# Optimization experiments

Measured on AMD Instinct MI355X. Metric: run time of the kernel, lower is better.

## Reference

```python
import jax, jax.numpy as jnp
import numpy as np

SCALE = 2.0   # init scale
OFFSET = 0.5  # init offset
BIG = 1e10    # stand-in for +inf so grads stay finite
N_PAD = 2048  # number of zero-padded pc columns per sample


def setup_inputs() -> dict:
    key = jax.random.key(0)
    k1, k2 = jax.random.split(key)
    vertices = jax.random.normal(k1, (4, 3, 64, 32, 64), dtype=jnp.float32)
    pc = jax.random.normal(k2, (4, 3, 8192), dtype=jnp.float32)
    # zero-pad the tail columns, mimicking variable-length point clouds
    pc = pc.at[:, :, 8192 - N_PAD:].set(0.0)
    return {"vertices": vertices, "pc": pc}


def _chamfer_loss(v, p, mask):
    # v: [N,3] mesh-top points; p: [M,3] cloud points; mask: [M] valid flags
    # squared pairwise distances via ||v||^2 + ||p||^2 - 2 v.p
    d = (jnp.sum(v * v, axis=1)[:, None]
         + jnp.sum(p * p, axis=1)[None, :]
         - 2.0 * (v @ p.T))                      # [N, M]
    dist1 = jnp.min(jnp.where(mask[None, :], d, BIG), axis=1)  # [N] v -> nearest valid p
    dist2 = jnp.min(d, axis=0)                                  # [M] p -> nearest v
    n_valid = jnp.maximum(jnp.sum(mask), 1).astype(d.dtype)
    return jnp.mean(dist1) + jnp.sum(jnp.where(mask, dist2, 0.0)) / n_valid


def reference(vertices, pc):
    B = vertices.shape[0]
    # top surface: last index along dim 3, flattened -> [B, 3, N]
    top = vertices[:, :, :, -1, :].reshape(B, 3, -1)
    top = (top - OFFSET) * SCALE
    v = jnp.transpose(top, (0, 2, 1))   # [B, N, 3]
    p = jnp.transpose(pc, (0, 2, 1))    # [B, M, 3]
    mask = ~jnp.all(pc == 0.0, axis=1)  # [B, M] valid (non-zero-padded) points
    loss = jax.vmap(_chamfer_loss)(v, p, mask)  # [B]
    return jnp.mean(loss)
```

## Files before the change

kernel.cpp:

```cpp
#include <hip/hip_runtime.h>

#define BATCH   4
#define NPTS    4096
#define MPTS    8192
#define TPB     256
#define VPT     8
#define MSPLIT  32
#define NSPLIT  16
#define MLEN    (MPTS / MSPLIT)
#define NLEN    (NPTS / NSPLIT)
#define D1_NBLK (NPTS / (TPB * VPT))
#define D2_MBLK (MPTS / (TPB * VPT))
#define D1_BLOCKS (BATCH * D1_NBLK * MSPLIT)
#define D2_BLOCKS (BATCH * D2_MBLK * NSPLIT)
#define BIGF    1.0e30f

#define PART1_ELEMS (MSPLIT * BATCH * NPTS)
#define PART2_ELEMS (NSPLIT * BATCH * MPTS)

#define R1_BLOCKS ((BATCH * NPTS) / (TPB * 4))
#define R2_BLOCKS ((BATCH * MPTS) / (TPB * 4))
#define R_BLOCKS  (R1_BLOCKS + R2_BLOCKS)

#define CTRL_FLOATS 16

__device__ __forceinline__ float vtop(const float* __restrict__ v, int b, int c, int n) {
    return v[b * 393216 + c * 131072 + ((n >> 6) << 11) + 1984 + (n & 63)];
}

__global__ void __launch_bounds__(TPB) dist_kernel(const float* __restrict__ vert,
                                                   const float* __restrict__ pc,
                                                   float* __restrict__ part1,
                                                   float* __restrict__ part2,
                                                   float* __restrict__ ctrl) {
    __shared__ float4 tile[TPB];
    const int tid = threadIdx.x;
    int blk = blockIdx.x;

    if (blk == 0 && tid < CTRL_FLOATS) ctrl[tid] = 0.0f;

    if (blk < D1_BLOCKS) {
        const int c  = blk % MSPLIT;
        const int nb = (blk / MSPLIT) % D1_NBLK;
        const int b  = blk / (MSPLIT * D1_NBLK);
        const float* pcb = pc + (size_t)b * 3 * MPTS;

        {
            const int m = c * MLEN + tid;
            const float qx = pcb[m], qy = pcb[MPTS + m], qz = pcb[2 * MPTS + m];
            const bool valid = !(qx == 0.0f && qy == 0.0f && qz == 0.0f);
            const float qn2 = valid ? 0.5f * (qx * qx + qy * qy + qz * qz) : BIGF;
            tile[tid] = make_float4(qx, qy, qz, qn2);
        }

        float vx[VPT], vy[VPT], vz[VPT], best[VPT];
        const int nbase = nb * (TPB * VPT) + tid;
#pragma unroll
        for (int k = 0; k < VPT; ++k) {
            const int n = nbase + k * TPB;
            vx[k] = (vtop(vert, b, 0, n) - 0.5f) * 2.0f;
            vy[k] = (vtop(vert, b, 1, n) - 0.5f) * 2.0f;
            vz[k] = (vtop(vert, b, 2, n) - 0.5f) * 2.0f;
            best[k] = BIGF;
        }
        __syncthreads();

#pragma unroll 4
        for (int j = 0; j < MLEN; ++j) {
            const float4 q = tile[j];
#pragma unroll
            for (int k = 0; k < VPT; ++k) {
                best[k] = fminf(best[k],
                    fmaf(-vx[k], q.x, fmaf(-vy[k], q.y, fmaf(-vz[k], q.z, q.w))));
            }
        }

        float* outp = part1 + (size_t)c * (BATCH * NPTS) + (size_t)b * NPTS;
#pragma unroll
        for (int k = 0; k < VPT; ++k) {
            const int n = nbase + k * TPB;
            const float vv = vx[k]*vx[k] + vy[k]*vy[k] + vz[k]*vz[k];
            outp[n] = fmaxf(vv + 2.0f * best[k], 0.0f);
        }
    } else {
        blk -= D1_BLOCKS;
        const int c  = blk % NSPLIT;
        const int mb = (blk / NSPLIT) % D2_MBLK;
        const int b  = blk / (NSPLIT * D2_MBLK);
        const float* pcb = pc + (size_t)b * 3 * MPTS;

        {
            const int n = c * NLEN + tid;
            const float sx = (vtop(vert, b, 0, n) - 0.5f) * 2.0f;
            const float sy = (vtop(vert, b, 1, n) - 0.5f) * 2.0f;
            const float sz = (vtop(vert, b, 2, n) - 0.5f) * 2.0f;
            tile[tid] = make_float4(sx, sy, sz, 0.5f * (sx*sx + sy*sy + sz*sz));
        }

        float qx[VPT], qy[VPT], qz[VPT], best[VPT];
        const int mbase = mb * (TPB * VPT) + tid;
#pragma unroll
        for (int k = 0; k < VPT; ++k) {
            const int m = mbase + k * TPB;
            qx[k] = pcb[m];
            qy[k] = pcb[MPTS + m];
            qz[k] = pcb[2 * MPTS + m];
            best[k] = BIGF;
        }
        __syncthreads();

#pragma unroll 4
        for (int j = 0; j < NLEN; ++j) {
            const float4 t = tile[j];
#pragma unroll
            for (int k = 0; k < VPT; ++k) {
                best[k] = fminf(best[k],
                    fmaf(-qx[k], t.x, fmaf(-qy[k], t.y, fmaf(-qz[k], t.z, t.w))));
            }
        }

        float* outp = part2 + (size_t)c * (BATCH * MPTS) + (size_t)b * MPTS;
#pragma unroll
        for (int k = 0; k < VPT; ++k) {
            const int m = mbase + k * TPB;
            const float qq = qx[k]*qx[k] + qy[k]*qy[k] + qz[k]*qz[k];
            outp[m] = fmaxf(qq + 2.0f * best[k], 0.0f);
        }
    }
}

__global__ void __launch_bounds__(TPB) reduce_kernel(const float* __restrict__ part1,
                                                     const float* __restrict__ part2,
                                                     const float* __restrict__ pc,
                                                     float* __restrict__ ctrl,
                                                     float* __restrict__ out) {
    const int tid = threadIdx.x;
    const int wid = tid >> 6;
    __shared__ float rs[4], rc[4];

    float s = 0.0f, cn = 0.0f;
    int b;

    if (blockIdx.x < R1_BLOCKS) {
        const int gid = blockIdx.x * (TPB * 4) + tid * 4;
        b = gid / NPTS;
        float4 best = make_float4(BIGF, BIGF, BIGF, BIGF);
#pragma unroll
        for (int c = 0; c < MSPLIT; ++c) {
            const float4 v = *(const float4*)&part1[(size_t)c * (BATCH * NPTS) + gid];
            best.x = fminf(best.x, v.x); best.y = fminf(best.y, v.y);
            best.z = fminf(best.z, v.z); best.w = fminf(best.w, v.w);
        }
        s = best.x + best.y + best.z + best.w;
    } else {
        const int g2 = (blockIdx.x - R1_BLOCKS) * (TPB * 4) + tid * 4;
        b = g2 / MPTS;
        const int m = g2 % MPTS;
        float4 best = make_float4(BIGF, BIGF, BIGF, BIGF);
#pragma unroll
        for (int c = 0; c < NSPLIT; ++c) {
            const float4 v = *(const float4*)&part2[(size_t)c * (BATCH * MPTS) + g2];
            best.x = fminf(best.x, v.x); best.y = fminf(best.y, v.y);
            best.z = fminf(best.z, v.z); best.w = fminf(best.w, v.w);
        }
        const float* pcb = pc + (size_t)b * 3 * MPTS;
        const float4 qx = *(const float4*)&pcb[m];
        const float4 qy = *(const float4*)&pcb[MPTS + m];
        const float4 qz = *(const float4*)&pcb[2 * MPTS + m];
        const bool v0 = !(qx.x == 0.0f && qy.x == 0.0f && qz.x == 0.0f);
        const bool v1 = !(qx.y == 0.0f && qy.y == 0.0f && qz.y == 0.0f);
        const bool v2 = !(qx.z == 0.0f && qy.z == 0.0f && qz.z == 0.0f);
        const bool v3 = !(qx.w == 0.0f && qy.w == 0.0f && qz.w == 0.0f);
        s  = (v0 ? best.x : 0.0f) + (v1 ? best.y : 0.0f)
           + (v2 ? best.z : 0.0f) + (v3 ? best.w : 0.0f);
        cn = (float)v0 + (float)v1 + (float)v2 + (float)v3;
    }

    for (int off = 32; off > 0; off >>= 1) {
        s  += __shfl_down(s, off, 64);
        cn += __shfl_down(cn, off, 64);
    }
    if ((tid & 63) == 0) { rs[wid] = s; rc[wid] = cn; }
    __syncthreads();

    if (tid == 0) {
        const float ts = rs[0] + rs[1] + rs[2] + rs[3];
        if (blockIdx.x < R1_BLOCKS) {
            atomicAdd(&ctrl[b], ts);
        } else {
            atomicAdd(&ctrl[4 + b], ts);
            atomicAdd(&ctrl[8 + b], rc[0] + rc[1] + rc[2] + rc[3]);
        }
        __threadfence();
        const unsigned int old = atomicAdd((unsigned int*)&ctrl[15], 1u);
        if (old == R_BLOCKS - 1) {
            float t = 0.0f;
            for (int bb = 0; bb < BATCH; ++bb) {
                const float s1 = atomicAdd(&ctrl[bb], 0.0f);
                const float s2 = atomicAdd(&ctrl[4 + bb], 0.0f);
                const float nv = atomicAdd(&ctrl[8 + bb], 0.0f);
                t += s1 * (1.0f / (float)NPTS) + s2 / fmaxf(nv, 1.0f);
            }
            out[0] = t * (1.0f / (float)BATCH);
        }
    }
}

extern "C" void kernel_launch(void* const* d_in, const int* in_sizes, int n_in,
                              void* d_out, int out_size, void* d_ws, size_t ws_size,
                              hipStream_t stream) {
    const float* vert = (const float*)d_in[0];
    const float* pc   = (const float*)d_in[1];
    float* out = (float*)d_out;

    float* part1 = (float*)d_ws;
    float* part2 = part1 + PART1_ELEMS;
    float* ctrl  = part2 + PART2_ELEMS;

    dist_kernel<<<D1_BLOCKS + D2_BLOCKS, TPB, 0, stream>>>(vert, pc, part1, part2, ctrl);
    reduce_kernel<<<R_BLOCKS, TPB, 0, stream>>>(part1, part2, pc, ctrl, out);
}
```

Baseline: 86.76 us.

## Use packed FP32 FMAs with larger per-thread tiles and smaller shared chunks

```diff
diff --git a/kernel.cpp b/kernel.cpp
--- a/kernel.cpp
+++ b/kernel.cpp
@@ -1,18 +1,17 @@
 #include <hip/hip_runtime.h>
+
+typedef float v2f __attribute__((ext_vector_type(2)));
 
 #define BATCH   4
 #define NPTS    4096
 #define MPTS    8192
 #define TPB     256
-#define VPT     8
-#define MSPLIT  32
-#define NSPLIT  16
-#define MLEN    (MPTS / MSPLIT)
-#define NLEN    (NPTS / NSPLIT)
-#define D1_NBLK (NPTS / (TPB * VPT))
-#define D2_MBLK (MPTS / (TPB * VPT))
-#define D1_BLOCKS (BATCH * D1_NBLK * MSPLIT)
-#define D2_BLOCKS (BATCH * D2_MBLK * NSPLIT)
+#define VPT     16
+#define CHUNK   128
+#define MSPLIT  (MPTS / CHUNK)
+#define NSPLIT  (NPTS / CHUNK)
+#define D1_BLOCKS (BATCH * MSPLIT)
+#define D2_BLOCKS (BATCH * 2 * NSPLIT)
 #define BIGF    1.0e30f
 
 #define PART1_ELEMS (MSPLIT * BATCH * NPTS)
@@ -28,103 +27,117 @@
     return v[b * 393216 + c * 131072 + ((n >> 6) << 11) + 1984 + (n & 63)];
 }
 
-__global__ void __launch_bounds__(TPB) dist_kernel(const float* __restrict__ vert,
-                                                   const float* __restrict__ pc,
-                                                   float* __restrict__ part1,
-                                                   float* __restrict__ part2,
-                                                   float* __restrict__ ctrl) {
-    __shared__ float4 tile[TPB];
+__device__ __forceinline__ void chunk_min(const float* __restrict__ sx,
+                                          const float* __restrict__ sy,
+                                          const float* __restrict__ sz,
+                                          const float* __restrict__ sw,
+                                          const v2f* __restrict__ ax,
+                                          const v2f* __restrict__ ay,
+                                          const v2f* __restrict__ az,
+                                          float* __restrict__ best) {
+#pragma unroll 2
+    for (int j = 0; j < CHUNK; j += 4) {
+        const float4 x4 = *(const float4*)&sx[j];
+        const float4 y4 = *(const float4*)&sy[j];
+        const float4 z4 = *(const float4*)&sz[j];
+        const float4 w4 = *(const float4*)&sw[j];
+        const v2f xa = {x4.x, x4.y}, xb = {x4.z, x4.w};
+        const v2f ya = {y4.x, y4.y}, yb = {y4.z, y4.w};
+        const v2f za = {z4.x, z4.y}, zb = {z4.z, z4.w};
+        const v2f wa = {w4.x, w4.y}, wb = {w4.z, w4.w};
+#pragma unroll
+        for (int k = 0; k < VPT; ++k) {
+            const v2f e0 = __builtin_elementwise_fma(ax[k], xa,
+                           __builtin_elementwise_fma(ay[k], ya,
+                           __builtin_elementwise_fma(az[k], za, wa)));
+            const v2f e1 = __builtin_elementwise_fma(ax[k], xb,
+                           __builtin_elementwise_fma(ay[k], yb,
+                           __builtin_elementwise_fma(az[k], zb, wb)));
+            best[k] = fminf(fminf(best[k], e0.x), e0.y);
+            best[k] = fminf(fminf(best[k], e1.x), e1.y);
+        }
+    }
+}
+
+__global__ void __launch_bounds__(TPB, 2) dist_kernel(const float* __restrict__ vert,
+                                                      const float* __restrict__ pc,
+                                                      float* __restrict__ part1,
+                                                      float* __restrict__ part2,
+                                                      float* __restrict__ ctrl) {
+    __shared__ __align__(16) float sx[CHUNK], sy[CHUNK], sz[CHUNK], sw[CHUNK];
     const int tid = threadIdx.x;
-    int blk = blockIdx.x;
+    const int blk = blockIdx.x;
 
     if (blk == 0 && tid < CTRL_FLOATS) ctrl[tid] = 0.0f;
 
+    v2f ax[VPT], ay[VPT], az[VPT];
+    float best[VPT];
+
     if (blk < D1_BLOCKS) {
-        const int c  = blk % MSPLIT;
-        const int nb = (blk / MSPLIT) % D1_NBLK;
-        const int b  = blk / (MSPLIT * D1_NBLK);
+        const int c = blk % MSPLIT;
+        const int b = blk / MSPLIT;
         const float* pcb = pc + (size_t)b * 3 * MPTS;
 
-        {
-            const int m = c * MLEN + tid;
+        if (tid < CHUNK) {
+            const int m = c * CHUNK + tid;
             const float qx = pcb[m], qy = pcb[MPTS + m], qz = pcb[2 * MPTS + m];
             const bool valid = !(qx == 0.0f && qy == 0.0f && qz == 0.0f);
-            const float qn2 = valid ? 0.5f * (qx * qx + qy * qy + qz * qz) : BIGF;
-            tile[tid] = make_float4(qx, qy, qz, qn2);
-        }
-
-        float vx[VPT], vy[VPT], vz[VPT], best[VPT];
-        const int nbase = nb * (TPB * VPT) + tid;
-#pragma unroll
-        for (int k = 0; k < VPT; ++k) {
-            const int n = nbase + k * TPB;
-            vx[k] = (vtop(vert, b, 0, n) - 0.5f) * 2.0f;
-            vy[k] = (vtop(vert, b, 1, n) - 0.5f) * 2.0f;
-            vz[k] = (vtop(vert, b, 2, n) - 0.5f) * 2.0f;
+            sx[tid] = qx; sy[tid] = qy; sz[tid] = qz;
+            sw[tid] = valid ? 0.5f * (qx * qx + qy * qy + qz * qz) : BIGF;
+        }
+#pragma unroll
+        for (int k = 0; k < VPT; ++k) {
+            const int n = k * TPB + tid;
+            const float x = (vtop(vert, b, 0, n) - 0.5f) * 2.0f;
+            const float y = (vtop(vert, b, 1, n) - 0.5f) * 2.0f;
+            const float z = (vtop(vert, b, 2, n) - 0.5f) * 2.0f;
+            ax[k] = (v2f){-x, -x}; ay[k] = (v2f){-y, -y}; az[k] = (v2f){-z, -z};
             best[k] = BIGF;
         }
         __syncthreads();
 
-#pragma unroll 4
-        for (int j = 0; j < MLEN; ++j) {
-            const float4 q = tile[j];
-#pragma unroll
-            for (int k = 0; k < VPT; ++k) {
-                best[k] = fminf(best[k],
-                    fmaf(-vx[k], q.x, fmaf(-vy[k], q.y, fmaf(-vz[k], q.z, q.w))));
-            }
-        }
+        chunk_min(sx, sy, sz, sw, ax, ay, az, best);
 
         float* outp = part1 + (size_t)c * (BATCH * NPTS) + (size_t)b * NPTS;
 #pragma unroll
         for (int k = 0; k < VPT; ++k) {
-            const int n = nbase + k * TPB;
-            const float vv = vx[k]*vx[k] + vy[k]*vy[k] + vz[k]*vz[k];
-            outp[n] = fmaxf(vv + 2.0f * best[k], 0.0f);
+            const int n = k * TPB + tid;
+            const float vv = ax[k].x * ax[k].x + ay[k].x * ay[k].x + az[k].x * az[k].x;
+            outp[n] = fmaxf(fmaf(2.0f, best[k], vv), 0.0f);
         }
     } else {
-        blk -= D1_BLOCKS;
-        const int c  = blk % NSPLIT;
-        const int mb = (blk / NSPLIT) % D2_MBLK;
-        const int b  = blk / (NSPLIT * D2_MBLK);
+        const int blk2 = blk - D1_BLOCKS;
+        const int c    = blk2 % NSPLIT;
+        const int half = (blk2 / NSPLIT) & 1;
+        const int b    = blk2 / (NSPLIT * 2);
         const float* pcb = pc + (size_t)b * 3 * MPTS;
 
-        {
-            const int n = c * NLEN + tid;
-            const float sx = (vtop(vert, b, 0, n) - 0.5f) * 2.0f;
-            const float sy = (vtop(vert, b, 1, n) - 0.5f) * 2.0f;
-            const float sz = (vtop(vert, b, 2, n) - 0.5f) * 2.0f;
-            tile[tid] = make_float4(sx, sy, sz, 0.5f * (sx*sx + sy*sy + sz*sz));
-        }
-
-        float qx[VPT], qy[VPT], qz[VPT], best[VPT];
-        const int mbase = mb * (TPB * VPT) + tid;
+        if (tid < CHUNK) {
+            const int n = c * CHUNK + tid;
+            const float x = (vtop(vert, b, 0, n) - 0.5f) * 2.0f;
+            const float y = (vtop(vert, b, 1, n) - 0.5f) * 2.0f;
+            const float z = (vtop(vert, b, 2, n) - 0.5f) * 2.0f;
+            sx[tid] = x; sy[tid] = y; sz[tid] = z;
+            sw[tid] = 0.5f * (x * x + y * y + z * z);
+        }
+        const int mbase = half * (TPB * VPT) + tid;
 #pragma unroll
         for (int k = 0; k < VPT; ++k) {
             const int m = mbase + k * TPB;
-            qx[k] = pcb[m];
-            qy[k] = pcb[MPTS + m];
-            qz[k] = pcb[2 * MPTS + m];
+            const float qx = pcb[m], qy = pcb[MPTS + m], qz = pcb[2 * MPTS + m];
+            ax[k] = (v2f){-qx, -qx}; ay[k] = (v2f){-qy, -qy}; az[k] = (v2f){-qz, -qz};
             best[k] = BIGF;
         }
         __syncthreads();
 
-#pragma unroll 4
-        for (int j = 0; j < NLEN; ++j) {
-            const float4 t = tile[j];
-#pragma unroll
-            for (int k = 0; k < VPT; ++k) {
-                best[k] = fminf(best[k],
-                    fmaf(-qx[k], t.x, fmaf(-qy[k], t.y, fmaf(-qz[k], t.z, t.w))));
-            }
-        }
+        chunk_min(sx, sy, sz, sw, ax, ay, az, best);
 
         float* outp = part2 + (size_t)c * (BATCH * MPTS) + (size_t)b * MPTS;
 #pragma unroll
         for (int k = 0; k < VPT; ++k) {
             const int m = mbase + k * TPB;
-            const float qq = qx[k]*qx[k] + qy[k]*qy[k] + qz[k]*qz[k];
-            outp[m] = fmaxf(qq + 2.0f * best[k], 0.0f);
+            const float qq = ax[k].x * ax[k].x + ay[k].x * ay[k].x + az[k].x * az[k].x;
+            outp[m] = fmaxf(fmaf(2.0f, best[k], qq), 0.0f);
         }
     }
 }
@@ -145,7 +158,7 @@
         const int gid = blockIdx.x * (TPB * 4) + tid * 4;
         b = gid / NPTS;
         float4 best = make_float4(BIGF, BIGF, BIGF, BIGF);
-#pragma unroll
+#pragma unroll 8
         for (int c = 0; c < MSPLIT; ++c) {
             const float4 v = *(const float4*)&part1[(size_t)c * (BATCH * NPTS) + gid];
             best.x = fminf(best.x, v.x); best.y = fminf(best.y, v.y);
@@ -157,7 +170,7 @@
         b = g2 / MPTS;
         const int m = g2 % MPTS;
         float4 best = make_float4(BIGF, BIGF, BIGF, BIGF);
-#pragma unroll
+#pragma unroll 8
         for (int c = 0; c < NSPLIT; ++c) {
             const float4 v = *(const float4*)&part2[(size_t)c * (BATCH * MPTS) + g2];
             best.x = fminf(best.x, v.x); best.y = fminf(best.y, v.y);
```

Measured after the change: 87.13 us. About the same (+0.4%).
